# Kernel optimization log

Hardware: AMD Instinct MI355X
Metric: run time of the kernel (lower is better)

Reference implementation:

```python
import jax, jax.numpy as jnp
import numpy as np

N = 100000   # nodes
E = 600000   # edges
IN = 128     # in_channels
H = 128      # hidden_channels
C = 47       # num_classes
L = 3        # num_layers
EPS = 1e-5   # batchnorm eps


def setup_inputs() -> dict:
    key = jax.random.key(0)
    ks = jax.random.split(key, 18)
    s = 0.05
    f = jnp.float32
    return {
        "x": jax.random.normal(ks[0], (N, IN), f),
        "in_W": jax.random.normal(ks[1], (IN, H), f) * s,
        "in_b": jnp.zeros((H,), f),
        "ibn_g": jnp.ones((H,), f),
        "ibn_b": jnp.zeros((H,), f),
        "ibn_m": jax.random.normal(ks[2], (H,), f) * 0.1,
        "ibn_v": jax.random.uniform(ks[3], (H,), f, 0.5, 1.5),
        "Wl": jax.random.normal(ks[4], (L, H, H), f) * s,   # SAGEConv lin_l (on aggregated neighbors)
        "bl": jnp.zeros((L, H), f),
        "Wr": jax.random.normal(ks[5], (L, H, H), f) * s,   # SAGEConv lin_r (root weight, no bias)
        "bn_g": jnp.ones((L, H), f),
        "bn_b": jnp.zeros((L, H), f),
        "bn_m": jax.random.normal(ks[6], (L, H), f) * 0.1,
        "bn_v": jax.random.uniform(ks[7], (L, H), f, 0.5, 1.5),
        "out_W": jax.random.normal(ks[8], (H, C), f) * s,
        "out_b": jnp.zeros((C,), f),
        "edge_index": jax.random.randint(ks[9], (2, E), 0, N),
    }


def _bn(h, g, b, m, v):
    # inference-mode BatchNorm1d with running stats
    return (h - m) * (g * jax.lax.rsqrt(v + EPS)) + b


def _sage(x, src, dst, Wl, bl, Wr):
    # mean aggregation of source features at destination nodes (PyG SAGEConv)
    msg = x[src]                                                   # [E, H] gather
    agg = jax.ops.segment_sum(msg, dst, num_segments=N)            # [N, H] scatter-add
    cnt = jax.ops.segment_sum(jnp.ones((src.shape[0],), x.dtype), dst, num_segments=N)
    agg = agg / jnp.maximum(cnt, 1.0)[:, None]                     # segment mean
    return agg @ Wl + bl + x @ Wr


def reference(x, in_W, in_b, ibn_g, ibn_b, ibn_m, ibn_v, Wl, bl, Wr,
              bn_g, bn_b, bn_m, bn_v, out_W, out_b, edge_index):
    src, dst = edge_index[0], edge_index[1]
    h = jax.nn.relu(_bn(x @ in_W + in_b, ibn_g, ibn_b, ibn_m, ibn_v))
    for l in range(L):  # small fixed layer count
        t = _sage(h, src, dst, Wl[l], bl[l], Wr[l])
        t = jax.nn.relu(_bn(t, bn_g[l], bn_b[l], bn_m[l], bn_v[l]))
        h = h + t  # residual
    return h @ out_W + out_b
```

## Files before the change

### kernel.cpp

```cpp
#include <hip/hip_runtime.h>
#include <math.h>

#define NN 100000
#define NE 600000
#define HD 128
#define NC 47
#define NL 3
#define BEPS 1e-5f

typedef unsigned short u16;
typedef unsigned int u32;
typedef __attribute__((ext_vector_type(8))) short bf16x8;
typedef __attribute__((ext_vector_type(4))) float f32x4;

__device__ inline u16 f2b(float f) {
  u32 u = __float_as_uint(f);
  u += 0x7fff + ((u >> 16) & 1);
  return (u16)(u >> 16);
}
__device__ inline float b2f(u16 us) { return __uint_as_float(((u32)us) << 16); }

__device__ inline void load_lds16(const void* g, void* l) {
  __builtin_amdgcn_global_load_lds(
      (const __attribute__((address_space(1))) void*)g,
      (__attribute__((address_space(3))) void*)l, 16, 0, 0);
}


__global__ void k_zero2(int* __restrict__ a, int* __restrict__ b) {
  int i = blockIdx.x * blockDim.x + threadIdx.x;
  if (i < NN) { a[i] = 0; b[i] = 0; }
}

#define DPG 12500

__global__ void k_hist(const int* __restrict__ dst, int* __restrict__ cnt) {
  int g = blockIdx.x & 7;
  int lo = g * DPG, hi = lo + DPG;
  int stride = (gridDim.x >> 3) * blockDim.x;
  for (int e = (blockIdx.x >> 3) * blockDim.x + threadIdx.x; e < NE; e += stride) {
    int d = dst[e];
    if (d >= lo && d < hi) atomicAdd(&cnt[d], 1);
  }
}

__global__ void k_scan1(const int* __restrict__ cnt, int* __restrict__ rs, int* __restrict__ part) {
  __shared__ int s[256];
  int tid = threadIdx.x;
  int base = blockIdx.x * 1024;
  int i0 = base + tid * 4;
  int c[4];
#pragma unroll
  for (int j = 0; j < 4; j++) c[j] = (i0 + j < NN) ? cnt[i0 + j] : 0;
  int tsum = c[0] + c[1] + c[2] + c[3];
  s[tid] = tsum;
  __syncthreads();
  for (int off = 1; off < 256; off <<= 1) {
    int v = (tid >= off) ? s[tid - off] : 0;
    __syncthreads();
    s[tid] += v;
    __syncthreads();
  }
  int run = s[tid] - tsum;
#pragma unroll
  for (int j = 0; j < 4; j++) {
    run += c[j];
    if (i0 + j < NN) rs[i0 + j + 1] = run;
  }
  if (tid == 255) part[blockIdx.x] = s[255];
}

__global__ void k_scan2(const int* __restrict__ part, int* __restrict__ offs, int nb, int* __restrict__ rs) {
  __shared__ int s[128];
  int tid = threadIdx.x;
  int v = (tid < nb) ? part[tid] : 0;
  s[tid] = v;
  __syncthreads();
  for (int off = 1; off < 128; off <<= 1) {
    int u = (tid >= off) ? s[tid - off] : 0;
    __syncthreads();
    s[tid] += u;
    __syncthreads();
  }
  if (tid < nb) offs[tid] = s[tid] - v;
  if (tid == 0) rs[0] = 0;
}

__global__ void k_scan3(int* __restrict__ rs, const int* __restrict__ offs) {
  int off = offs[blockIdx.x];
  int base = blockIdx.x * 1024;
  int tid = threadIdx.x;
#pragma unroll
  for (int j = 0; j < 4; j++) {
    int i = base + tid * 4 + j;
    if (i < NN) rs[i + 1] += off;
  }
}

__global__ void k_scatter(const int* __restrict__ src, const int* __restrict__ dstA,
                          const int* __restrict__ rs, int* __restrict__ cur, int* __restrict__ ssrc) {
  int g = blockIdx.x & 7;
  int lo = g * DPG, hi = lo + DPG;
  int stride = (gridDim.x >> 3) * blockDim.x;
  for (int e = (blockIdx.x >> 3) * blockDim.x + threadIdx.x; e < NE; e += stride) {
    int d = dstA[e];
    if (d >= lo && d < hi) {
      int p = atomicAdd(&cur[d], 1);
      ssrc[rs[d] + p] = src[e];
    }
  }
}


__global__ void k_pack_all(const float* __restrict__ inW, const float* __restrict__ Wl,
                           const float* __restrict__ Wr, const float* __restrict__ oW,
                           u16* __restrict__ wpin, u16* __restrict__ wpl, u16* __restrict__ wpo) {
  int bid = blockIdx.x;
  int lane = threadIdx.x;
  int g = lane >> 4, r = lane & 15;
  union { u16 u[8]; uint4 v; } o;
  if (bid < 32) {
    int kt = bid >> 3, nt = bid & 7;
#pragma unroll
    for (int j = 0; j < 8; j++) {
      int k = kt * 32 + g * 8 + j, n = nt * 16 + r;
      o.u[j] = f2b(inW[k * HD + n]);
    }
    *(uint4*)(wpin + ((size_t)bid * 64 + lane) * 8) = o.v;
  } else if (bid < 224) {
    int b2 = bid - 32;
    int l = b2 >> 6, T = b2 & 63;
    int kt = T >> 3, nt = T & 7;
    const float* wl = Wl + (size_t)l * HD * HD;
    const float* wr = Wr + (size_t)l * HD * HD;
#pragma unroll
    for (int j = 0; j < 8; j++) {
      int k = kt * 32 + g * 8 + j, n = nt * 16 + r;
      o.u[j] = f2b(k < HD ? wl[k * HD + n] : wr[(k - HD) * HD + n]);
    }
    *(uint4*)(wpl + (((size_t)l * 64 + T) * 64 + lane) * 8) = o.v;
  } else {
    int T = bid - 224;
    int kt = T / 3, nt = T % 3;
#pragma unroll
    for (int j = 0; j < 8; j++) {
      int k = kt * 32 + g * 8 + j, n = nt * 16 + r;
      o.u[j] = (n < NC) ? f2b(oW[k * NC + n]) : (u16)0;
    }
    *(uint4*)(wpo + ((size_t)T * 64 + lane) * 8) = o.v;
  }
}


__global__ void k_agg(const u16* __restrict__ h, const int* __restrict__ rs,
                      const int* __restrict__ ssrc, u16* __restrict__ agg) {
  int gw = (blockIdx.x * blockDim.x + threadIdx.x) >> 6;
  int lane = threadIdx.x & 63;
  if (gw >= NN) return;
  int s = rs[gw], e = rs[gw + 1];
  const u32* h32 = (const u32*)h;
  float a0 = 0.f, a1 = 0.f;
  if (e > s) {
    for (int p = s; p < e; p += 8) {
      int rem = e - p;
      int idx[8];
#pragma unroll
      for (int j = 0; j < 8; j++) idx[j] = ssrc[p + min(j, rem - 1)];
      u32 u[8];
#pragma unroll
      for (int j = 0; j < 8; j++) u[j] = h32[(size_t)idx[j] * 64 + lane];
#pragma unroll
      for (int j = 0; j < 8; j++) {
        float msk = (j < rem) ? 1.0f : 0.0f;
        a0 += msk * b2f((u16)(u[j] & 0xffff));
        a1 += msk * b2f((u16)(u[j] >> 16));
      }
    }
  }
  float inv = 1.0f / (float)max(e - s, 1);
  u32 o = (u32)f2b(a0 * inv) | ((u32)f2b(a1 * inv) << 16);
  ((u32*)agg)[(size_t)gw * 64 + lane] = o;
}


template <int KS, int MODE>
__global__ __launch_bounds__(256, 4) void k_mm(
    const float* __restrict__ Af, const u16* __restrict__ A0, const u16* __restrict__ A1,
    const u16* __restrict__ Wp, u16* __restrict__ hout,
    const float* __restrict__ bias, const float* __restrict__ g,
    const float* __restrict__ bb, const float* __restrict__ m,
    const float* __restrict__ v) {
  __shared__ __align__(1024) char As_raw[64 * KS * 64];
  __shared__ float sc_s[HD], sh_s[HD];
  int tid = threadIdx.x;
  int lane = tid & 63;
  int w = tid >> 6;
  long rbase = (long)blockIdx.x * 64;

  if (tid < HD) {
    float sc = g[tid] * rsqrtf(v[tid] + BEPS);
    sc_s[tid] = sc;
    sh_s[tid] = (bias[tid] - m[tid]) * sc + bb[tid];
  }

  if constexpr (MODE == 1) {
#pragma unroll
    for (int t = 0; t < 8; t++) {
      int op = w * 8 + t;
      int rowL = op * 2 + (lane >> 5);
      int p = lane & 31;
      int q = (p & 16) | ((p & 15) ^ (rowL & 15));
      long rg = rbase + rowL; if (rg > NN - 1) rg = NN - 1;
      const char* src = (q < 16)
          ? (const char*)A0 + rg * 256 + (size_t)q * 16
          : (const char*)A1 + rg * 256 + (size_t)(q - 16) * 16;
      load_lds16(src, As_raw + (size_t)op * 1024);
    }
  } else {
    int row = tid >> 2;
    int cq = (tid & 3) * 4;
    long rg = rbase + row; if (rg > NN - 1) rg = NN - 1;
    const float* srcp = Af + rg * HD + cq * 8;
#pragma unroll
    for (int ch = 0; ch < 4; ch++) {
      float4 f0 = *(const float4*)(srcp + ch * 8);
      float4 f1 = *(const float4*)(srcp + ch * 8 + 4);
      union { u16 u[8]; uint4 v4; } o;
      o.u[0] = f2b(f0.x); o.u[1] = f2b(f0.y); o.u[2] = f2b(f0.z); o.u[3] = f2b(f0.w);
      o.u[4] = f2b(f1.x); o.u[5] = f2b(f1.y); o.u[6] = f2b(f1.z); o.u[7] = f2b(f1.w);
      int q = cq + ch;
      int p = q ^ (row & 15);
      *(uint4*)(As_raw + (size_t)row * 256 + (size_t)p * 16) = o.v4;
    }
  }
  __syncthreads();

  int nb = w * 32;
  f32x4 acc[4][2];
#pragma unroll
  for (int mi = 0; mi < 4; mi++)
#pragma unroll
    for (int ni = 0; ni < 2; ni++) acc[mi][ni] = (f32x4)(0.0f);

#pragma unroll
  for (int kt = 0; kt < KS; kt++) {
    bf16x8 bfr[2];
#pragma unroll
    for (int ni = 0; ni < 2; ni++)
      bfr[ni] = *(const bf16x8*)(Wp + (((size_t)kt * 8 + (w * 2 + ni)) * 64 + lane) * 8);
#pragma unroll
    for (int mi = 0; mi < 4; mi++) {
      int row = mi * 16 + (lane & 15);
      int slot = kt * 4 + (lane >> 4);
      int p = (slot & ~15) | ((slot & 15) ^ (row & 15));
      bf16x8 afr = *(const bf16x8*)(As_raw + (size_t)row * (KS * 64) + (size_t)p * 16);
#pragma unroll
      for (int ni = 0; ni < 2; ni++)
        acc[mi][ni] = __builtin_amdgcn_mfma_f32_16x16x32_bf16(afr, bfr[ni], acc[mi][ni], 0, 0, 0);
    }
  }

#pragma unroll
  for (int mi = 0; mi < 4; mi++) {
#pragma unroll
    for (int ni = 0; ni < 2; ni++) {
      int c = nb + ni * 16 + (lane & 15);
      float sc = sc_s[c], sh = sh_s[c];
#pragma unroll
      for (int r = 0; r < 4; r++) {
        int rowL = mi * 16 + (lane >> 4) * 4 + r;
        long rg = rbase + rowL;
        if (rg >= NN) continue;
        float val = fmaxf(acc[mi][ni][r] * sc + sh, 0.f);
        if constexpr (MODE == 1) {
          int p = 16 | ((c >> 3) ^ (rowL & 15));
          u16 ho = *(const u16*)(As_raw + (size_t)rowL * 512 + (size_t)p * 16 + (c & 7) * 2);
          val += b2f(ho);
        }
        hout[rg * HD + c] = f2b(val);
      }
    }
  }
}


__global__ __launch_bounds__(256, 4) void k_outmm(const u16* __restrict__ h,
                                                  const u16* __restrict__ Wp,
                                                  const float* __restrict__ ob,
                                                  float* __restrict__ outp) {
  __shared__ __align__(1024) char As_raw[64 * 256];
  int tid = threadIdx.x;
  int lane = tid & 63;
  int w = tid >> 6;
  long rbase = (long)blockIdx.x * 64;
#pragma unroll
  for (int t = 0; t < 4; t++) {
    int op = w * 4 + t;
    int rowL = op * 4 + (lane >> 4);
    int p = lane & 15;
    int q = p ^ (rowL & 15);
    long rg = rbase + rowL; if (rg > NN - 1) rg = NN - 1;
    load_lds16((const char*)h + rg * 256 + (size_t)q * 16, As_raw + (size_t)op * 1024);
  }
  __syncthreads();

  f32x4 acc[3];
#pragma unroll
  for (int nt = 0; nt < 3; nt++) acc[nt] = (f32x4)(0.0f);
  int rowb = w * 16;
#pragma unroll
  for (int kt = 0; kt < 4; kt++) {
    int row = rowb + (lane & 15);
    int slot = kt * 4 + (lane >> 4);
    int p = slot ^ (row & 15);
    bf16x8 afr = *(const bf16x8*)(As_raw + (size_t)row * 256 + (size_t)p * 16);
#pragma unroll
    for (int nt = 0; nt < 3; nt++) {
      bf16x8 bfr = *(const bf16x8*)(Wp + (((size_t)kt * 3 + nt) * 64 + lane) * 8);
      acc[nt] = __builtin_amdgcn_mfma_f32_16x16x32_bf16(afr, bfr, acc[nt], 0, 0, 0);
    }
  }
#pragma unroll
  for (int nt = 0; nt < 3; nt++) {
#pragma unroll
    for (int r = 0; r < 4; r++) {
      long rg = rbase + rowb + (lane >> 4) * 4 + r;
      int c = nt * 16 + (lane & 15);
      if (rg < NN && c < NC) outp[rg * NC + c] = acc[nt][r] + ob[c];
    }
  }
}


extern "C" void kernel_launch(void* const* d_in, const int* in_sizes, int n_in,
                              void* d_out, int out_size, void* d_ws, size_t ws_size,
                              hipStream_t stream) {
  const float* x     = (const float*)d_in[0];
  const float* in_W  = (const float*)d_in[1];
  const float* in_b  = (const float*)d_in[2];
  const float* ibn_g = (const float*)d_in[3];
  const float* ibn_b = (const float*)d_in[4];
  const float* ibn_m = (const float*)d_in[5];
  const float* ibn_v = (const float*)d_in[6];
  const float* Wl    = (const float*)d_in[7];
  const float* bl    = (const float*)d_in[8];
  const float* Wr    = (const float*)d_in[9];
  const float* bn_g  = (const float*)d_in[10];
  const float* bn_b  = (const float*)d_in[11];
  const float* bn_m  = (const float*)d_in[12];
  const float* bn_v  = (const float*)d_in[13];
  const float* oW    = (const float*)d_in[14];
  const float* ob    = (const float*)d_in[15];
  const int* ei      = (const int*)d_in[16];
  const int* srcA = ei;
  const int* dstA = ei + NE;
  float* outp = (float*)d_out;

  char* W = (char*)d_ws;
  u16* h    = (u16*)W;
  u16* agg  = (u16*)(W + 25600000);
  u16* wpin = (u16*)(W + 76800000);
  u16* wpl  = (u16*)(W + 76800000 + 32768);
  u16* wpo  = (u16*)(W + 76800000 + 32768 + 196608);
  int* rs   = (int*)(W + 77041664);
  int* cnt  = rs + (NN + 1);
  int* cur  = cnt + NN;
  int* ssrc = cur + NN;
  int* part = ssrc + NE;
  int* offs = part + 128;

  k_zero2<<<(NN + 255) / 256, 256, 0, stream>>>(cnt, cur);
  k_hist<<<2048, 256, 0, stream>>>(dstA, cnt);
  int nb1 = (NN + 1023) / 1024;
  k_scan1<<<nb1, 256, 0, stream>>>(cnt, rs, part);
  k_scan2<<<1, 128, 0, stream>>>(part, offs, nb1, rs);
  k_scan3<<<nb1, 256, 0, stream>>>(rs, offs);
  k_scatter<<<2048, 256, 0, stream>>>(srcA, dstA, rs, cur, ssrc);

  k_pack_all<<<236, 64, 0, stream>>>(in_W, Wl, Wr, oW, wpin, wpl, wpo);

  int gblocks = (NN + 63) / 64;
  k_mm<4, 0><<<gblocks, 256, 0, stream>>>(x, nullptr, nullptr, wpin, h,
                                          in_b, ibn_g, ibn_b, ibn_m, ibn_v);
  for (int l = 0; l < NL; ++l) {
    k_agg<<<NN / 4, 256, 0, stream>>>(h, rs, ssrc, agg);
    k_mm<8, 1><<<gblocks, 256, 0, stream>>>(nullptr, agg, h, wpl + (size_t)l * 64 * 512, h,
                                            bl + (size_t)l * HD, bn_g + (size_t)l * HD,
                                            bn_b + (size_t)l * HD, bn_m + (size_t)l * HD,
                                            bn_v + (size_t)l * HD);
  }
  k_outmm<<<gblocks, 256, 0, stream>>>(h, wpo, ob, outp);
}
```

Baseline: 368.4 us.

## Fuse neighbor mean aggregation into SAGE matmul kernel with ping-pong h buffers

Removes the separate aggregation kernel: each matmul block now gathers and averages neighbor rows for its 64 nodes directly into LDS, then runs the MFMA matmul on the concatenated aggregate and root features. This avoids writing and re-reading the intermediate aggregate array and saves one launch per layer. Because the fused kernel reads h for other rows while writing outputs, it ping-pongs between two h buffers. The cost is lower gather parallelism per block, since each wave walks 16 rows serially, and the gather latency now runs inside the matmul kernel under its launch bounds.

```diff
diff --git a/kernel.cpp b/kernel.cpp
--- a/kernel.cpp
+++ b/kernel.cpp
@@ -152,45 +152,15 @@
 }
 
 
-__global__ void k_agg(const u16* __restrict__ h, const int* __restrict__ rs,
-                      const int* __restrict__ ssrc, u16* __restrict__ agg) {
-  int gw = (blockIdx.x * blockDim.x + threadIdx.x) >> 6;
-  int lane = threadIdx.x & 63;
-  if (gw >= NN) return;
-  int s = rs[gw], e = rs[gw + 1];
-  const u32* h32 = (const u32*)h;
-  float a0 = 0.f, a1 = 0.f;
-  if (e > s) {
-    for (int p = s; p < e; p += 8) {
-      int rem = e - p;
-      int idx[8];
-#pragma unroll
-      for (int j = 0; j < 8; j++) idx[j] = ssrc[p + min(j, rem - 1)];
-      u32 u[8];
-#pragma unroll
-      for (int j = 0; j < 8; j++) u[j] = h32[(size_t)idx[j] * 64 + lane];
-#pragma unroll
-      for (int j = 0; j < 8; j++) {
-        float msk = (j < rem) ? 1.0f : 0.0f;
-        a0 += msk * b2f((u16)(u[j] & 0xffff));
-        a1 += msk * b2f((u16)(u[j] >> 16));
-      }
-    }
-  }
-  float inv = 1.0f / (float)max(e - s, 1);
-  u32 o = (u32)f2b(a0 * inv) | ((u32)f2b(a1 * inv) << 16);
-  ((u32*)agg)[(size_t)gw * 64 + lane] = o;
-}
-
-
 template <int KS, int MODE>
 __global__ __launch_bounds__(256, 4) void k_mm(
-    const float* __restrict__ Af, const u16* __restrict__ A0, const u16* __restrict__ A1,
+    const float* __restrict__ Af, const u16* __restrict__ Ah,
+    const int* __restrict__ rs, const int* __restrict__ ssrc,
     const u16* __restrict__ Wp, u16* __restrict__ hout,
     const float* __restrict__ bias, const float* __restrict__ g,
     const float* __restrict__ bb, const float* __restrict__ m,
     const float* __restrict__ v) {
-  __shared__ __align__(1024) char As_raw[64 * KS * 64];
+  __shared__ __align__(1024) char As_raw[(KS == 8) ? 32768 : 16384];
   __shared__ float sc_s[HD], sh_s[HD];
   int tid = threadIdx.x;
   int lane = tid & 63;
@@ -205,16 +175,45 @@
 
   if constexpr (MODE == 1) {
 #pragma unroll
-    for (int t = 0; t < 8; t++) {
-      int op = w * 8 + t;
-      int rowL = op * 2 + (lane >> 5);
-      int p = lane & 31;
-      int q = (p & 16) | ((p & 15) ^ (rowL & 15));
+    for (int t = 0; t < 4; t++) {
+      int op = w * 4 + t;
+      int rowL = op * 4 + (lane >> 4);
+      int p = lane & 15;
+      int q = p ^ (rowL & 15);
       long rg = rbase + rowL; if (rg > NN - 1) rg = NN - 1;
-      const char* src = (q < 16)
-          ? (const char*)A0 + rg * 256 + (size_t)q * 16
-          : (const char*)A1 + rg * 256 + (size_t)(q - 16) * 16;
-      load_lds16(src, As_raw + (size_t)op * 1024);
+      load_lds16((const char*)Ah + rg * 256 + (size_t)q * 16,
+                 As_raw + 16384 + (size_t)op * 1024);
+    }
+    const u32* h32 = (const u32*)Ah;
+    for (int i = 0; i < 16; i++) {
+      int r = w * 16 + i;
+      long n = rbase + r;
+      float a0 = 0.f, a1 = 0.f;
+      float inv = 1.0f;
+      if (n < NN) {
+        int s = rs[n], e = rs[n + 1];
+        if (e > s) {
+          for (int pp = s; pp < e; pp += 8) {
+            int rem = e - pp;
+            int idx[8];
+#pragma unroll
+            for (int j = 0; j < 8; j++) idx[j] = ssrc[pp + min(j, rem - 1)];
+            u32 u[8];
+#pragma unroll
+            for (int j = 0; j < 8; j++) u[j] = h32[(size_t)idx[j] * 64 + lane];
+#pragma unroll
+            for (int j = 0; j < 8; j++) {
+              float msk = (j < rem) ? 1.0f : 0.0f;
+              a0 += msk * b2f((u16)(u[j] & 0xffff));
+              a1 += msk * b2f((u16)(u[j] >> 16));
+            }
+          }
+          inv = 1.0f / (float)(e - s);
+        }
+      }
+      u32 o = (u32)f2b(a0 * inv) | ((u32)f2b(a1 * inv) << 16);
+      int chunk = (lane >> 2) ^ (r & 15);
+      *(u32*)(As_raw + (size_t)r * 256 + (size_t)chunk * 16 + (lane & 3) * 4) = o;
     }
   } else {
     int row = tid >> 2;
@@ -235,7 +234,7 @@
   }
   __syncthreads();
 
-  int nb = w * 32;
+  int nbase = w * 32;
   f32x4 acc[4][2];
 #pragma unroll
   for (int mi = 0; mi < 4; mi++)
@@ -252,8 +251,8 @@
     for (int mi = 0; mi < 4; mi++) {
       int row = mi * 16 + (lane & 15);
       int slot = kt * 4 + (lane >> 4);
-      int p = (slot & ~15) | ((slot & 15) ^ (row & 15));
-      bf16x8 afr = *(const bf16x8*)(As_raw + (size_t)row * (KS * 64) + (size_t)p * 16);
+      int addr = ((slot & 16) << 10) + row * 256 + (((slot & 15) ^ (row & 15)) << 4);
+      bf16x8 afr = *(const bf16x8*)(As_raw + addr);
 #pragma unroll
       for (int ni = 0; ni < 2; ni++)
         acc[mi][ni] = __builtin_amdgcn_mfma_f32_16x16x32_bf16(afr, bfr[ni], acc[mi][ni], 0, 0, 0);
@@ -264,7 +263,7 @@
   for (int mi = 0; mi < 4; mi++) {
 #pragma unroll
     for (int ni = 0; ni < 2; ni++) {
-      int c = nb + ni * 16 + (lane & 15);
+      int c = nbase + ni * 16 + (lane & 15);
       float sc = sc_s[c], sh = sh_s[c];
 #pragma unroll
       for (int r = 0; r < 4; r++) {
@@ -273,9 +272,8 @@
         if (rg >= NN) continue;
         float val = fmaxf(acc[mi][ni][r] * sc + sh, 0.f);
         if constexpr (MODE == 1) {
-          int p = 16 | ((c >> 3) ^ (rowL & 15));
-          u16 ho = *(const u16*)(As_raw + (size_t)rowL * 512 + (size_t)p * 16 + (c & 7) * 2);
-          val += b2f(ho);
+          int addr = 16384 + rowL * 256 + ((((c >> 3) ^ (rowL & 15))) << 4) + (c & 7) * 2;
+          val += b2f(*(const u16*)(As_raw + addr));
         }
         hout[rg * HD + c] = f2b(val);
       }
@@ -358,7 +356,7 @@
 
   char* W = (char*)d_ws;
   u16* h    = (u16*)W;
-  u16* agg  = (u16*)(W + 25600000);
+  u16* h2   = (u16*)(W + 25600000);
   u16* wpin = (u16*)(W + 76800000);
   u16* wpl  = (u16*)(W + 76800000 + 32768);
   u16* wpo  = (u16*)(W + 76800000 + 32768 + 196608);
@@ -380,14 +378,17 @@
   k_pack_all<<<236, 64, 0, stream>>>(in_W, Wl, Wr, oW, wpin, wpl, wpo);
 
   int gblocks = (NN + 63) / 64;
-  k_mm<4, 0><<<gblocks, 256, 0, stream>>>(x, nullptr, nullptr, wpin, h,
+  k_mm<4, 0><<<gblocks, 256, 0, stream>>>(x, nullptr, nullptr, nullptr, wpin, h,
                                           in_b, ibn_g, ibn_b, ibn_m, ibn_v);
+  u16* hin = h;
+  u16* hout = h2;
   for (int l = 0; l < NL; ++l) {
-    k_agg<<<NN / 4, 256, 0, stream>>>(h, rs, ssrc, agg);
-    k_mm<8, 1><<<gblocks, 256, 0, stream>>>(nullptr, agg, h, wpl + (size_t)l * 64 * 512, h,
+    k_mm<8, 1><<<gblocks, 256, 0, stream>>>(nullptr, hin, rs, ssrc,
+                                            wpl + (size_t)l * 64 * 512, hout,
                                             bl + (size_t)l * HD, bn_g + (size_t)l * HD,
                                             bn_b + (size_t)l * HD, bn_m + (size_t)l * HD,
                                             bn_v + (size_t)l * HD);
-  }
-  k_outmm<<<gblocks, 256, 0, stream>>>(h, wpo, ob, outp);
-}
+    u16* t = hin; hin = hout; hout = t;
+  }
+  k_outmm<<<gblocks, 256, 0, stream>>>(hin, wpo, ob, outp);
+}
```

Result: slower. 394.5 us (+7.1%).
